# Kernel tuning notes

Measured on AMD Instinct MI355X. Metric: run time of the kernel, lower is better.

Reference implementation:

```python
import jax, jax.numpy as jnp
import numpy as np


def _adder2d(x, w, stride, padding):
    """AdderNet 'convolution': out[b,o,i,j] = -sum_p |patch[b,p,i,j] - w[o,p]|.

    x: [B, C, H, W], w: [O, C, kh, kw]. Patches are extracted in (C, kh, kw)
    channel-major order, matching torch.nn.functional.unfold / w.reshape(O, -1).
    """
    O, C, kh, kw = w.shape
    patches = jax.lax.conv_general_dilated_patches(
        x, (kh, kw), (stride, stride), [(padding, padding), (padding, padding)])
    B, P, Ho, Wo = patches.shape  # P = C*kh*kw
    p = patches.reshape(B, P, Ho * Wo)
    wf = w.reshape(O, P)

    def per_out(wo):  # sequential over small O to avoid a [B,O,P,L] blowup
        return -jnp.sum(jnp.abs(p - wo[None, :, None]), axis=1)  # [B, L]

    out = jax.lax.map(per_out, wf)  # [O, B, L]
    return jnp.transpose(out, (1, 0, 2)).reshape(B, O, Ho, Wo)


def setup_inputs() -> dict:
    key = jax.random.key(0)
    ks = jax.random.split(key, 5)
    x = jax.random.normal(ks[0], (4096, 1, 28, 28), dtype=jnp.float32)
    w1 = jax.random.normal(ks[1], (16, 1, 3, 3), dtype=jnp.float32)
    w2 = jax.random.normal(ks[2], (32, 16, 3, 3), dtype=jnp.float32)
    w3 = jax.random.normal(ks[3], (16, 32, 3, 3), dtype=jnp.float32)
    w4 = jax.random.normal(ks[4], (10, 16, 3, 3), dtype=jnp.float32)
    return {"x": x, "w1": w1, "w2": w2, "w3": w3, "w4": w4}


def reference(x, w1, w2, w3, w4):
    h = x - 0.5
    h = jax.nn.relu((_adder2d(h, w1, 2, 0) + 10.0) / 4.0)   # [B,16,13,13]
    h = jax.nn.relu((_adder2d(h, w2, 2, 1) + 130.0) / 8.0)  # [B,32,7,7]
    h = jax.nn.relu((_adder2d(h, w3, 2, 1) + 280.0) / 16.0)  # [B,16,4,4]
    h = _adder2d(h, w4, 2, 0)                                # [B,10,1,1]
    h = h.reshape(h.shape[0], -1)                            # [B,10]
    return jax.nn.log_softmax(h, axis=1)
```

## Files before the change

kernel.cpp:

```cpp
#include <hip/hip_runtime.h>
#include <math.h>


#if defined(__has_builtin)
#if __has_builtin(__builtin_amdgcn_sad_u16)
#define HAS_SAD 1
#endif
#endif

__device__ __forceinline__ unsigned sadu16(unsigned a, unsigned b, unsigned acc) {
#ifdef HAS_SAD
  return __builtin_amdgcn_sad_u16(a, b, acc);
#else
  int al = (int)(a & 0xFFFFu), ah = (int)(a >> 16);
  int bl = (int)(b & 0xFFFFu), bh = (int)(b >> 16);
  return acc + (unsigned)(al > bl ? al - bl : bl - al)
             + (unsigned)(ah > bh ? ah - bh : bh - ah);
#endif
}

__device__ __forceinline__ unsigned quant(float v) {
  return (unsigned)fmaf(v, 1024.0f, 8192.5f);
}
__device__ __forceinline__ unsigned quantx(float v) {
  return (unsigned)fmaf(v, 1024.0f, 7680.5f);
}
__device__ __forceinline__ int imax(int a, int b) { return a > b ? a : b; }

#define QPAD 0x20002000u

__global__ void adder_prep(const float* __restrict__ w1, const float* __restrict__ w2,
                           const float* __restrict__ w3, const float* __restrict__ w4,
                           unsigned* __restrict__ qw) {
  int k = blockIdx.x * 256 + threadIdx.x;
  if (k < 96) {
    int o = k / 6, r = k % 6, kh = r >> 1, h = r & 1;
    const float* p = w1 + o * 9 + kh * 3;
    qw[k] = h ? quant(p[2]) : (quant(p[0]) | (quant(p[1]) << 16));
  } else if (k < 2400) {
    int k2 = k - 96, m = k2 / 288, r = k2 % 288, o = r / 9, pk = r % 9;
    int s = o * 144 + 2 * m * 9 + pk;
    qw[k] = quant(w2[s]) | (quant(w2[s + 9]) << 16);
  } else if (k < 4704) {
    int k3 = k - 2400, m2 = k3 / 144, r = k3 % 144, o = r / 9, pk = r % 9;
    int s = o * 288 + 2 * m2 * 9 + pk;
    qw[k] = quant(w3[s]) | (quant(w3[s + 9]) << 16);
  } else if (k < 5424) {
    int k4 = k - 4704, m = k4 / 90, r = k4 % 90, o = r / 9, pk = r % 9;
    int s = o * 144 + 2 * m * 9 + pk;
    qw[k] = quant(w4[s]) | (quant(w4[s + 9]) << 16);
  }
}

__global__ __launch_bounds__(64, 4) void adder_main(
    const float* __restrict__ gx,
    const unsigned* __restrict__ qw,
    float* __restrict__ gout)
{
  __shared__ __align__(16) unsigned sA1[1352];
  __shared__ __align__(16) unsigned sA2[784];

  const int t = threadIdx.x;
  const int b = blockIdx.x;
  const float* img = gx + (size_t)b * 784;

  if (t < 52) {
    const int i = t >> 2, jq = t & 3;
    unsigned r[3][5], mw[3][4];
#pragma unroll
    for (int kh = 0; kh < 3; ++kh) {
      const float* rp = img + (2 * i + kh) * 28 + 8 * jq;
      float4 A = *(const float4*)(rp);
      float4 B = *(const float4*)(rp + 4);
      float2 C = *(const float2*)(rp + 8);
      r[kh][0] = quantx(A.x) | (quantx(A.y) << 16);
      r[kh][1] = quantx(A.z) | (quantx(A.w) << 16);
      r[kh][2] = quantx(B.x) | (quantx(B.y) << 16);
      r[kh][3] = quantx(B.z) | (quantx(B.w) << 16);
      r[kh][4] = quantx(C.x) | (quantx(C.y) << 16);
#pragma unroll
      for (int c = 0; c < 4; ++c) mw[kh][c] = r[kh][c + 1] & 0xFFFFu;
    }
#pragma unroll 1
    for (int op = 0; op < 8; ++op) {
      const unsigned* w = qw + op * 12;
      unsigned a0[4], a1[4];
#pragma unroll
      for (int jj = 0; jj < 4; ++jj) { a0[jj] = 0u; a1[jj] = 0u; }
#pragma unroll
      for (int kh = 0; kh < 3; ++kh) {
        unsigned wa01 = w[kh * 2], wa2 = w[kh * 2 + 1];
        unsigned wb01 = w[6 + kh * 2], wb2 = w[6 + kh * 2 + 1];
#pragma unroll
        for (int jj = 0; jj < 4; ++jj) {
          a0[jj] = sadu16(r[kh][jj], wa01, a0[jj]);
          a0[jj] = sadu16(mw[kh][jj], wa2, a0[jj]);
          a1[jj] = sadu16(r[kh][jj], wb01, a1[jj]);
          a1[jj] = sadu16(mw[kh][jj], wb2, a1[jj]);
        }
      }
      unsigned* dst = sA1 + op * 169 + i * 13 + 4 * jq;
#pragma unroll
      for (int jj = 0; jj < 4; ++jj) {
        if (4 * jq + jj < 13) {
          int q0 = imax(10752 - (int)((a0[jj] + 2u) >> 2), 8192);
          int q1 = imax(10752 - (int)((a1[jj] + 2u) >> 2), 8192);
          dst[jj] = (unsigned)q0 | ((unsigned)q1 << 16);
        }
      }
    }
  }
  __syncthreads();

  if (t < 49) {
    const int i = t / 7, j = t % 7;
    int ro[3], co[3];
    bool rv[3], cv[3];
#pragma unroll
    for (int k = 0; k < 3; ++k) {
      int r = 2 * i - 1 + k;
      rv[k] = (r >= 0) && (r < 13);
      ro[k] = rv[k] ? r * 13 : 0;
      int c = 2 * j - 1 + k;
      cv[k] = (c >= 0) && (c < 13);
      co[k] = cv[k] ? c : 0;
    }
    unsigned acc[32];
#pragma unroll
    for (int o = 0; o < 32; ++o) acc[o] = 0u;
    const unsigned* qw2 = qw + 96;
#pragma unroll 2
    for (int m = 0; m < 8; ++m) {
      const unsigned* plane = sA1 + m * 169;
      unsigned p[3][3];
#pragma unroll
      for (int kh = 0; kh < 3; ++kh)
#pragma unroll
        for (int c = 0; c < 3; ++c) {
          unsigned v = plane[ro[kh] + co[c]];
          p[kh][c] = (rv[kh] && cv[c]) ? v : QPAD;
        }
      const unsigned* wm = qw2 + m * 288;
#pragma unroll
      for (int o = 0; o < 32; ++o) {
        const unsigned* w9 = wm + o * 9;
        unsigned a = acc[o];
#pragma unroll
        for (int kh = 0; kh < 3; ++kh)
#pragma unroll
          for (int c = 0; c < 3; ++c)
            a = sadu16(p[kh][c], w9[kh * 3 + c], a);
        acc[o] = a;
      }
    }
#pragma unroll
    for (int m2 = 0; m2 < 16; ++m2) {
      int q0 = imax(24832 - (int)((acc[2 * m2] + 4u) >> 3), 8192);
      int q1 = imax(24832 - (int)((acc[2 * m2 + 1] + 4u) >> 3), 8192);
      sA2[m2 * 49 + i * 7 + j] = (unsigned)q0 | ((unsigned)q1 << 16);
    }
  }
  __syncthreads();

  {
    const int pos = t & 15, og = (t >> 4) & 1, mg = t >> 5;
    const int i = pos >> 2, j = pos & 3;
    int ro[3], co[3];
    bool rv[3], cv[3];
#pragma unroll
    for (int k = 0; k < 3; ++k) {
      int r = 2 * i - 1 + k;
      rv[k] = (r >= 0) && (r < 7);
      ro[k] = rv[k] ? r * 7 : 0;
      int c = 2 * j - 1 + k;
      cv[k] = (c >= 0) && (c < 7);
      co[k] = cv[k] ? c : 0;
    }
    unsigned acc[8];
#pragma unroll
    for (int o = 0; o < 8; ++o) acc[o] = 0u;
    const unsigned* qw3 = qw + 2400;
#pragma unroll 2
    for (int mm = 0; mm < 8; ++mm) {
      const int m2 = mg * 8 + mm;
      const unsigned* plane = sA2 + m2 * 49;
      unsigned p[3][3];
#pragma unroll
      for (int kh = 0; kh < 3; ++kh)
#pragma unroll
        for (int c = 0; c < 3; ++c) {
          unsigned v = plane[ro[kh] + co[c]];
          p[kh][c] = (rv[kh] && cv[c]) ? v : QPAD;
        }
      const unsigned* ws = qw3 + m2 * 144 + og * 72;
#pragma unroll
      for (int oo = 0; oo < 8; ++oo) {
        const unsigned* w9 = ws + oo * 9;
        unsigned a = acc[oo];
#pragma unroll
        for (int kh = 0; kh < 3; ++kh)
#pragma unroll
          for (int c = 0; c < 3; ++c)
            a = sadu16(p[kh][c], w9[kh * 3 + c], a);
        acc[oo] = a;
      }
    }
    unsigned* pp = sA1 + t * 12;
    *(uint4*)(pp)     = make_uint4(acc[0], acc[1], acc[2], acc[3]);
    *(uint4*)(pp + 4) = make_uint4(acc[4], acc[5], acc[6], acc[7]);
  }
  __syncthreads();

  if (t < 16) {
    const int pos = t;
#pragma unroll
    for (int m = 0; m < 8; ++m) {
      const int og = m >> 2, oo = 2 * (m & 3);
      const int b0 = (og * 16 + pos) * 12;
      unsigned s0 = sA1[b0 + oo]     + sA1[b0 + 384 + oo];
      unsigned s1 = sA1[b0 + oo + 1] + sA1[b0 + 384 + oo + 1];
      int q0 = imax(26112 - (int)((s0 + 8u) >> 4), 8192);
      int q1 = imax(26112 - (int)((s1 + 8u) >> 4), 8192);
      sA1[800 + m * 17 + pos] = (unsigned)q0 | ((unsigned)q1 << 16);
    }
  }
  __syncthreads();

  if (t < 40) {
    const int o = t % 10, mq = t / 10;
    const unsigned* qw4 = qw + 4704;
    unsigned acc = 0u;
#pragma unroll
    for (int mm = 0; mm < 2; ++mm) {
      const int m = mq * 2 + mm;
      const unsigned* a3 = sA1 + 800 + m * 17;
      const unsigned* w9 = qw4 + (m * 10 + o) * 9;
#pragma unroll
      for (int kh = 0; kh < 3; ++kh)
#pragma unroll
        for (int kw = 0; kw < 3; ++kw)
          acc = sadu16(a3[kh * 4 + kw], w9[kh * 3 + kw], acc);
    }
    sA1[940 + t] = acc;
  }
  __syncthreads();
  if (t < 10) {
    unsigned s = sA1[940 + t] + sA1[950 + t] + sA1[960 + t] + sA1[970 + t];
    ((float*)sA1)[980 + t] = -(float)s * (1.0f / 1024.0f);
  }
  __syncthreads();
  if (t < 10) {
    const float* lg = (const float*)sA1 + 980;
    float mx = lg[0];
#pragma unroll
    for (int k = 1; k < 10; ++k) mx = fmaxf(mx, lg[k]);
    float sum = 0.0f;
#pragma unroll
    for (int k = 0; k < 10; ++k) sum += __expf(lg[k] - mx);
    gout[(size_t)b * 10 + t] = lg[t] - mx - __logf(sum);
  }
}

extern "C" void kernel_launch(void* const* d_in, const int* in_sizes, int n_in,
                              void* d_out, int out_size, void* d_ws, size_t ws_size,
                              hipStream_t stream) {
  const float* x  = (const float*)d_in[0];
  const float* w1 = (const float*)d_in[1];
  const float* w2 = (const float*)d_in[2];
  const float* w3 = (const float*)d_in[3];
  const float* w4 = (const float*)d_in[4];
  unsigned* qw = (unsigned*)d_ws;
  float* out = (float*)d_out;
  adder_prep<<<22, 256, 0, stream>>>(w1, w2, w3, w4, qw);
  adder_main<<<4096, 64, 0, stream>>>(x, qw, out);
}
```

Baseline: 127.9 us.

## Split each image's adder layers across two waves per block

Each block now has 128 threads, and the two wavefronts split the per-image work. In layer 1 they take halves of the output planes, in layer 2 halves of the output channels, and in layer 3 halves of the outputs with the input channels split further across lane groups. The layer-3 partial reduction and the final layer are rearranged to match: eight partial sums per logit instead of four, with shared-memory offsets moved. This shortens the serial dependency chain per block and cuts per-thread accumulator registers, so more waves can hide latency. The cost is more partial-sum reduction and block synchronisation shared between two waves.

```diff
diff --git a/kernel.cpp b/kernel.cpp
--- a/kernel.cpp
+++ b/kernel.cpp
@@ -52,7 +52,7 @@
   }
 }
 
-__global__ __launch_bounds__(64, 4) void adder_main(
+__global__ __launch_bounds__(128, 8) void adder_main(
     const float* __restrict__ gx,
     const unsigned* __restrict__ qw,
     float* __restrict__ gout)
@@ -61,11 +61,13 @@
   __shared__ __align__(16) unsigned sA2[784];
 
   const int t = threadIdx.x;
+  const int wave = t >> 6;
+  const int lane = t & 63;
   const int b = blockIdx.x;
   const float* img = gx + (size_t)b * 784;
 
-  if (t < 52) {
-    const int i = t >> 2, jq = t & 3;
+  if (lane < 52) {
+    const int i = lane >> 2, jq = lane & 3;
     unsigned r[3][5], mw[3][4];
 #pragma unroll
     for (int kh = 0; kh < 3; ++kh) {
@@ -82,7 +84,8 @@
       for (int c = 0; c < 4; ++c) mw[kh][c] = r[kh][c + 1] & 0xFFFFu;
     }
 #pragma unroll 1
-    for (int op = 0; op < 8; ++op) {
+    for (int opl = 0; opl < 4; ++opl) {
+      const int op = wave * 4 + opl;
       const unsigned* w = qw + op * 12;
       unsigned a0[4], a1[4];
 #pragma unroll
@@ -112,8 +115,8 @@
   }
   __syncthreads();
 
-  if (t < 49) {
-    const int i = t / 7, j = t % 7;
+  if (lane < 49) {
+    const int i = lane / 7, j = lane % 7;
     int ro[3], co[3];
     bool rv[3], cv[3];
 #pragma unroll
@@ -125,11 +128,11 @@
       cv[k] = (c >= 0) && (c < 13);
       co[k] = cv[k] ? c : 0;
     }
-    unsigned acc[32];
-#pragma unroll
-    for (int o = 0; o < 32; ++o) acc[o] = 0u;
-    const unsigned* qw2 = qw + 96;
-#pragma unroll 2
+    unsigned acc[16];
+#pragma unroll
+    for (int o = 0; o < 16; ++o) acc[o] = 0u;
+    const unsigned* qw2 = qw + 96 + wave * 144;
+#pragma unroll 1
     for (int m = 0; m < 8; ++m) {
       const unsigned* plane = sA1 + m * 169;
       unsigned p[3][3];
@@ -142,7 +145,7 @@
         }
       const unsigned* wm = qw2 + m * 288;
 #pragma unroll
-      for (int o = 0; o < 32; ++o) {
+      for (int o = 0; o < 16; ++o) {
         const unsigned* w9 = wm + o * 9;
         unsigned a = acc[o];
 #pragma unroll
@@ -154,16 +157,16 @@
       }
     }
 #pragma unroll
-    for (int m2 = 0; m2 < 16; ++m2) {
+    for (int m2 = 0; m2 < 8; ++m2) {
       int q0 = imax(24832 - (int)((acc[2 * m2] + 4u) >> 3), 8192);
       int q1 = imax(24832 - (int)((acc[2 * m2 + 1] + 4u) >> 3), 8192);
-      sA2[m2 * 49 + i * 7 + j] = (unsigned)q0 | ((unsigned)q1 << 16);
+      sA2[(wave * 8 + m2) * 49 + i * 7 + j] = (unsigned)q0 | ((unsigned)q1 << 16);
     }
   }
   __syncthreads();
 
   {
-    const int pos = t & 15, og = (t >> 4) & 1, mg = t >> 5;
+    const int pos = lane & 15, mg = lane >> 4;
     const int i = pos >> 2, j = pos & 3;
     int ro[3], co[3];
     bool rv[3], cv[3];
@@ -180,9 +183,9 @@
 #pragma unroll
     for (int o = 0; o < 8; ++o) acc[o] = 0u;
     const unsigned* qw3 = qw + 2400;
-#pragma unroll 2
-    for (int mm = 0; mm < 8; ++mm) {
-      const int m2 = mg * 8 + mm;
+#pragma unroll 1
+    for (int mm = 0; mm < 4; ++mm) {
+      const int m2 = mg * 4 + mm;
       const unsigned* plane = sA2 + m2 * 49;
       unsigned p[3][3];
 #pragma unroll
@@ -192,7 +195,7 @@
           unsigned v = plane[ro[kh] + co[c]];
           p[kh][c] = (rv[kh] && cv[c]) ? v : QPAD;
         }
-      const unsigned* ws = qw3 + m2 * 144 + og * 72;
+      const unsigned* ws = qw3 + m2 * 144 + wave * 72;
 #pragma unroll
       for (int oo = 0; oo < 8; ++oo) {
         const unsigned* w9 = ws + oo * 9;
@@ -205,7 +208,7 @@
         acc[oo] = a;
       }
     }
-    unsigned* pp = sA1 + t * 12;
+    unsigned* pp = sA1 + t * 8;
     *(uint4*)(pp)     = make_uint4(acc[0], acc[1], acc[2], acc[3]);
     *(uint4*)(pp + 4) = make_uint4(acc[4], acc[5], acc[6], acc[7]);
   }
@@ -216,41 +219,43 @@
 #pragma unroll
     for (int m = 0; m < 8; ++m) {
       const int og = m >> 2, oo = 2 * (m & 3);
-      const int b0 = (og * 16 + pos) * 12;
-      unsigned s0 = sA1[b0 + oo]     + sA1[b0 + 384 + oo];
-      unsigned s1 = sA1[b0 + oo + 1] + sA1[b0 + 384 + oo + 1];
+      unsigned s0 = 0u, s1 = 0u;
+#pragma unroll
+      for (int mg = 0; mg < 4; ++mg) {
+        const int base = (og * 64 + mg * 16 + pos) * 8;
+        s0 += sA1[base + oo];
+        s1 += sA1[base + oo + 1];
+      }
       int q0 = imax(26112 - (int)((s0 + 8u) >> 4), 8192);
       int q1 = imax(26112 - (int)((s1 + 8u) >> 4), 8192);
-      sA1[800 + m * 17 + pos] = (unsigned)q0 | ((unsigned)q1 << 16);
-    }
-  }
-  __syncthreads();
-
-  if (t < 40) {
+      sA1[1100 + m * 17 + pos] = (unsigned)q0 | ((unsigned)q1 << 16);
+    }
+  }
+  __syncthreads();
+
+  if (t < 80) {
     const int o = t % 10, mq = t / 10;
     const unsigned* qw4 = qw + 4704;
+    const unsigned* a3 = sA1 + 1100 + mq * 17;
+    const unsigned* w9 = qw4 + (mq * 10 + o) * 9;
     unsigned acc = 0u;
 #pragma unroll
-    for (int mm = 0; mm < 2; ++mm) {
-      const int m = mq * 2 + mm;
-      const unsigned* a3 = sA1 + 800 + m * 17;
-      const unsigned* w9 = qw4 + (m * 10 + o) * 9;
-#pragma unroll
-      for (int kh = 0; kh < 3; ++kh)
-#pragma unroll
-        for (int kw = 0; kw < 3; ++kw)
-          acc = sadu16(a3[kh * 4 + kw], w9[kh * 3 + kw], acc);
-    }
-    sA1[940 + t] = acc;
+    for (int kh = 0; kh < 3; ++kh)
+#pragma unroll
+      for (int kw = 0; kw < 3; ++kw)
+        acc = sadu16(a3[kh * 4 + kw], w9[kh * 3 + kw], acc);
+    sA1[1240 + t] = acc;
   }
   __syncthreads();
   if (t < 10) {
-    unsigned s = sA1[940 + t] + sA1[950 + t] + sA1[960 + t] + sA1[970 + t];
-    ((float*)sA1)[980 + t] = -(float)s * (1.0f / 1024.0f);
+    unsigned s = 0u;
+#pragma unroll
+    for (int mq = 0; mq < 8; ++mq) s += sA1[1240 + mq * 10 + t];
+    ((float*)sA1)[1280 + t] = -(float)s * (1.0f / 1024.0f);
   }
   __syncthreads();
   if (t < 10) {
-    const float* lg = (const float*)sA1 + 980;
+    const float* lg = (const float*)sA1 + 1280;
     float mx = lg[0];
 #pragma unroll
     for (int k = 1; k < 10; ++k) mx = fmaxf(mx, lg[k]);
@@ -272,5 +277,5 @@
   unsigned* qw = (unsigned*)d_ws;
   float* out = (float*)d_out;
   adder_prep<<<22, 256, 0, stream>>>(w1, w2, w3, w4, qw);
-  adder_main<<<4096, 64, 0, stream>>>(x, qw, out);
-}
+  adder_main<<<4096, 128, 0, stream>>>(x, qw, out);
+}
```

Measured after the change: 154.8 us. 21.1% more time.

## Cache input patches in registers and loop over outputs in adder layers 2-3

Applied to the files above, without the earlier changes.

Layers 2 and 3 now load all eight input-channel 3x3 patches into registers once. They then iterate over output channels with several independent SAD accumulators, instead of reloading patches per channel and keeping 32 or 8 accumulators live. The weight packing is reordered to be output-major so each output's weights are contiguous. The layer-3 partial-sum layout in shared memory and the offsets for later stages are changed to match, and layer 1's op loop is unrolled by 2. This trades accumulator registers for patch registers and adds accumulator ILP, which may change register pressure and occupancy.

```diff
diff --git a/kernel.cpp b/kernel.cpp
--- a/kernel.cpp
+++ b/kernel.cpp
@@ -38,11 +38,11 @@
     const float* p = w1 + o * 9 + kh * 3;
     qw[k] = h ? quant(p[2]) : (quant(p[0]) | (quant(p[1]) << 16));
   } else if (k < 2400) {
-    int k2 = k - 96, m = k2 / 288, r = k2 % 288, o = r / 9, pk = r % 9;
+    int k2 = k - 96, o = k2 / 72, r = k2 % 72, m = r / 9, pk = r % 9;
     int s = o * 144 + 2 * m * 9 + pk;
     qw[k] = quant(w2[s]) | (quant(w2[s + 9]) << 16);
   } else if (k < 4704) {
-    int k3 = k - 2400, m2 = k3 / 144, r = k3 % 144, o = r / 9, pk = r % 9;
+    int k3 = k - 2400, o = k3 / 144, r = k3 % 144, m2 = r / 9, pk = r % 9;
     int s = o * 288 + 2 * m2 * 9 + pk;
     qw[k] = quant(w3[s]) | (quant(w3[s + 9]) << 16);
   } else if (k < 5424) {
@@ -81,7 +81,7 @@
 #pragma unroll
       for (int c = 0; c < 4; ++c) mw[kh][c] = r[kh][c + 1] & 0xFFFFu;
     }
-#pragma unroll 1
+#pragma unroll 2
     for (int op = 0; op < 8; ++op) {
       const unsigned* w = qw + op * 12;
       unsigned a0[4], a1[4];
@@ -114,50 +114,48 @@
 
   if (t < 49) {
     const int i = t / 7, j = t % 7;
-    int ro[3], co[3];
-    bool rv[3], cv[3];
-#pragma unroll
-    for (int k = 0; k < 3; ++k) {
-      int r = 2 * i - 1 + k;
-      rv[k] = (r >= 0) && (r < 13);
-      ro[k] = rv[k] ? r * 13 : 0;
-      int c = 2 * j - 1 + k;
-      cv[k] = (c >= 0) && (c < 13);
-      co[k] = cv[k] ? c : 0;
-    }
-    unsigned acc[32];
-#pragma unroll
-    for (int o = 0; o < 32; ++o) acc[o] = 0u;
-    const unsigned* qw2 = qw + 96;
-#pragma unroll 2
+    int off[9];
+    bool val[9];
+#pragma unroll
+    for (int kh = 0; kh < 3; ++kh) {
+      int rr = 2 * i - 1 + kh;
+      bool rvv = (rr >= 0) && (rr < 13);
+      int roo = rvv ? rr * 13 : 0;
+#pragma unroll
+      for (int c = 0; c < 3; ++c) {
+        int cc = 2 * j - 1 + c;
+        bool cvv = (cc >= 0) && (cc < 13);
+        val[kh * 3 + c] = rvv && cvv;
+        off[kh * 3 + c] = roo + (cvv ? cc : 0);
+      }
+    }
+    unsigned p[8][9];
+#pragma unroll
     for (int m = 0; m < 8; ++m) {
       const unsigned* plane = sA1 + m * 169;
-      unsigned p[3][3];
-#pragma unroll
-      for (int kh = 0; kh < 3; ++kh)
-#pragma unroll
-        for (int c = 0; c < 3; ++c) {
-          unsigned v = plane[ro[kh] + co[c]];
-          p[kh][c] = (rv[kh] && cv[c]) ? v : QPAD;
-        }
-      const unsigned* wm = qw2 + m * 288;
-#pragma unroll
-      for (int o = 0; o < 32; ++o) {
-        const unsigned* w9 = wm + o * 9;
-        unsigned a = acc[o];
-#pragma unroll
-        for (int kh = 0; kh < 3; ++kh)
-#pragma unroll
-          for (int c = 0; c < 3; ++c)
-            a = sadu16(p[kh][c], w9[kh * 3 + c], a);
-        acc[o] = a;
-      }
-    }
-#pragma unroll
-    for (int m2 = 0; m2 < 16; ++m2) {
-      int q0 = imax(24832 - (int)((acc[2 * m2] + 4u) >> 3), 8192);
-      int q1 = imax(24832 - (int)((acc[2 * m2 + 1] + 4u) >> 3), 8192);
-      sA2[m2 * 49 + i * 7 + j] = (unsigned)q0 | ((unsigned)q1 << 16);
+#pragma unroll
+      for (int k = 0; k < 9; ++k) {
+        unsigned v = plane[off[k]];
+        p[m][k] = val[k] ? v : QPAD;
+      }
+    }
+#pragma unroll 2
+    for (int o2 = 0; o2 < 16; ++o2) {
+      const unsigned* w = qw + 96 + o2 * 144;
+      unsigned aA0 = 0u, aA1 = 0u, aB0 = 0u, aB1 = 0u;
+#pragma unroll
+      for (int m = 0; m < 4; ++m)
+#pragma unroll
+        for (int k = 0; k < 9; ++k) {
+          aA0 = sadu16(p[m][k],     w[m * 9 + k],       aA0);
+          aA1 = sadu16(p[m + 4][k], w[36 + m * 9 + k],  aA1);
+          aB0 = sadu16(p[m][k],     w[72 + m * 9 + k],  aB0);
+          aB1 = sadu16(p[m + 4][k], w[108 + m * 9 + k], aB1);
+        }
+      unsigned SA = aA0 + aA1, SB = aB0 + aB1;
+      int q0 = imax(24832 - (int)((SA + 4u) >> 3), 8192);
+      int q1 = imax(24832 - (int)((SB + 4u) >> 3), 8192);
+      sA2[o2 * 49 + i * 7 + j] = (unsigned)q0 | ((unsigned)q1 << 16);
     }
   }
   __syncthreads();
@@ -165,49 +163,44 @@
   {
     const int pos = t & 15, og = (t >> 4) & 1, mg = t >> 5;
     const int i = pos >> 2, j = pos & 3;
-    int ro[3], co[3];
-    bool rv[3], cv[3];
-#pragma unroll
-    for (int k = 0; k < 3; ++k) {
-      int r = 2 * i - 1 + k;
-      rv[k] = (r >= 0) && (r < 7);
-      ro[k] = rv[k] ? r * 7 : 0;
-      int c = 2 * j - 1 + k;
-      cv[k] = (c >= 0) && (c < 7);
-      co[k] = cv[k] ? c : 0;
-    }
-    unsigned acc[8];
-#pragma unroll
-    for (int o = 0; o < 8; ++o) acc[o] = 0u;
-    const unsigned* qw3 = qw + 2400;
+    int off[9];
+    bool val[9];
+#pragma unroll
+    for (int kh = 0; kh < 3; ++kh) {
+      int rr = 2 * i - 1 + kh;
+      bool rvv = (rr >= 0) && (rr < 7);
+      int roo = rvv ? rr * 7 : 0;
+#pragma unroll
+      for (int c = 0; c < 3; ++c) {
+        int cc = 2 * j - 1 + c;
+        bool cvv = (cc >= 0) && (cc < 7);
+        val[kh * 3 + c] = rvv && cvv;
+        off[kh * 3 + c] = roo + (cvv ? cc : 0);
+      }
+    }
+    unsigned p[8][9];
+#pragma unroll
+    for (int mm = 0; mm < 8; ++mm) {
+      const unsigned* plane = sA2 + (mg * 8 + mm) * 49;
+#pragma unroll
+      for (int k = 0; k < 9; ++k) {
+        unsigned v = plane[off[k]];
+        p[mm][k] = val[k] ? v : QPAD;
+      }
+    }
 #pragma unroll 2
-    for (int mm = 0; mm < 8; ++mm) {
-      const int m2 = mg * 8 + mm;
-      const unsigned* plane = sA2 + m2 * 49;
-      unsigned p[3][3];
-#pragma unroll
-      for (int kh = 0; kh < 3; ++kh)
-#pragma unroll
-        for (int c = 0; c < 3; ++c) {
-          unsigned v = plane[ro[kh] + co[c]];
-          p[kh][c] = (rv[kh] && cv[c]) ? v : QPAD;
-        }
-      const unsigned* ws = qw3 + m2 * 144 + og * 72;
-#pragma unroll
-      for (int oo = 0; oo < 8; ++oo) {
-        const unsigned* w9 = ws + oo * 9;
-        unsigned a = acc[oo];
-#pragma unroll
-        for (int kh = 0; kh < 3; ++kh)
-#pragma unroll
-          for (int c = 0; c < 3; ++c)
-            a = sadu16(p[kh][c], w9[kh * 3 + c], a);
-        acc[oo] = a;
-      }
-    }
-    unsigned* pp = sA1 + t * 12;
-    *(uint4*)(pp)     = make_uint4(acc[0], acc[1], acc[2], acc[3]);
-    *(uint4*)(pp + 4) = make_uint4(acc[4], acc[5], acc[6], acc[7]);
+    for (int oo = 0; oo < 8; ++oo) {
+      const unsigned* w = qw + 2400 + (og * 8 + oo) * 144 + mg * 72;
+      unsigned a0 = 0u, a1 = 0u;
+#pragma unroll
+      for (int mm = 0; mm < 4; ++mm)
+#pragma unroll
+        for (int k = 0; k < 9; ++k) {
+          a0 = sadu16(p[mm][k],     w[mm * 9 + k],      a0);
+          a1 = sadu16(p[mm + 4][k], w[36 + mm * 9 + k], a1);
+        }
+      sA1[((og * 8 + oo) * 16 + pos) * 2 + mg] = a0 + a1;
+    }
   }
   __syncthreads();
 
@@ -215,13 +208,13 @@
     const int pos = t;
 #pragma unroll
     for (int m = 0; m < 8; ++m) {
-      const int og = m >> 2, oo = 2 * (m & 3);
-      const int b0 = (og * 16 + pos) * 12;
-      unsigned s0 = sA1[b0 + oo]     + sA1[b0 + 384 + oo];
-      unsigned s1 = sA1[b0 + oo + 1] + sA1[b0 + 384 + oo + 1];
+      const int b0 = (2 * m * 16 + pos) * 2;
+      const int b1 = ((2 * m + 1) * 16 + pos) * 2;
+      unsigned s0 = sA1[b0] + sA1[b0 + 1];
+      unsigned s1 = sA1[b1] + sA1[b1 + 1];
       int q0 = imax(26112 - (int)((s0 + 8u) >> 4), 8192);
       int q1 = imax(26112 - (int)((s1 + 8u) >> 4), 8192);
-      sA1[800 + m * 17 + pos] = (unsigned)q0 | ((unsigned)q1 << 16);
+      sA1[1100 + m * 17 + pos] = (unsigned)q0 | ((unsigned)q1 << 16);
     }
   }
   __syncthreads();
@@ -233,7 +226,7 @@
 #pragma unroll
     for (int mm = 0; mm < 2; ++mm) {
       const int m = mq * 2 + mm;
-      const unsigned* a3 = sA1 + 800 + m * 17;
+      const unsigned* a3 = sA1 + 1100 + m * 17;
       const unsigned* w9 = qw4 + (m * 10 + o) * 9;
 #pragma unroll
       for (int kh = 0; kh < 3; ++kh)
@@ -241,16 +234,16 @@
         for (int kw = 0; kw < 3; ++kw)
           acc = sadu16(a3[kh * 4 + kw], w9[kh * 3 + kw], acc);
     }
-    sA1[940 + t] = acc;
+    sA1[1240 + t] = acc;
   }
   __syncthreads();
   if (t < 10) {
-    unsigned s = sA1[940 + t] + sA1[950 + t] + sA1[960 + t] + sA1[970 + t];
-    ((float*)sA1)[980 + t] = -(float)s * (1.0f / 1024.0f);
+    unsigned s = sA1[1240 + t] + sA1[1250 + t] + sA1[1260 + t] + sA1[1270 + t];
+    ((float*)sA1)[1280 + t] = -(float)s * (1.0f / 1024.0f);
   }
   __syncthreads();
   if (t < 10) {
-    const float* lg = (const float*)sA1 + 980;
+    const float* lg = (const float*)sA1 + 1280;
     float mx = lg[0];
 #pragma unroll
     for (int k = 1; k < 10; ++k) mx = fmaxf(mx, lg[k]);
```

Result: faster. 118.9 us (-7.0%).
